# Kernel optimization log

Hardware: AMD Instinct MI355X
Metric: run time of the kernel (lower is better)

Reference implementation:

```python
import jax, jax.numpy as jnp
import numpy as np

# GraphVToS (keras) faithful jax reference.
# Original math: for every atom pair (i,j), concat(vf[i], vf[j]) along features,
# project with w_vs [2F,K] + b_vs, multiply by pairwise distance vector d[i,j,c],
# sum over coordinate axis c (=3), apply activation.
# We avoid materializing the [B,N,N,3,2F] tile by splitting w_vs into the halves
# acting on vf[i] and vf[j] (exact same linear map, distributivity of concat-matmul).

B, N, C, F, K = 8, 128, 3, 64, 64

def setup_inputs() -> dict:
    key = jax.random.key(0)
    k1, k2, k3 = jax.random.split(key, 3)
    vector_features = jax.random.normal(k1, (B, N, C, F), dtype=jnp.float32)
    distances = jax.random.normal(k2, (B, N, N, C), dtype=jnp.float32)
    w_vs = jax.random.normal(k3, (2 * F, K), dtype=jnp.float32) * (1.0 / np.sqrt(2 * F))
    b_vs = jnp.zeros((K,), dtype=jnp.float32)
    return {"vector_features": vector_features, "distances": distances,
            "w_vs": w_vs, "b_vs": b_vs}

def reference(vector_features, distances, w_vs, b_vs):
    f = vector_features.shape[-1]
    w_i, w_j = w_vs[:f], w_vs[f:]          # halves acting on vf[i] / vf[j]
    # Per-atom projections: [B,N,C,K]
    p_i = jnp.einsum('bncf,fk->bnck', vector_features, w_i)
    p_j = jnp.einsum('bncf,fk->bnck', vector_features, w_j)
    # Distance-weighted reduction over coordinate axis c -> [B,N,N,K]
    s = (jnp.einsum('bick,bijc->bijk', p_i, distances)
         + jnp.einsum('bjck,bijc->bijk', p_j, distances))
    # Bias contributes b_vs * sum_c d[i,j,c]
    s = s + distances.sum(axis=-1)[..., None] * b_vs
    return jax.nn.relu(s)
```

## Files before the change

kernel.cpp:

```cpp
#include <hip/hip_runtime.h>

#define Bz 8
#define Nz 128
#define Cz 3
#define Fz 64
#define Kz 64

__global__ __launch_bounds__(256) void proj_kernel(const float* __restrict__ vf,
                                                   const float4* __restrict__ w4,
                                                   const float4* __restrict__ bv4,
                                                   float4* __restrict__ P4) {
    int idx = blockIdx.x * blockDim.x + threadIdx.x;
    const int PER4 = (Bz * Nz * Cz * Kz) / 4;
    int which = idx / PER4;
    int rem   = idx - which * PER4;
    int k4 = rem & 15;
    int c  = (rem >> 4) % Cz;
    int bn = rem / (Cz * Kz / 4);

    const float*  vrow = vf + (bn * Cz + c) * Fz;
    const float4* wcol = w4 + which * (Fz * Kz / 4) + k4;

    float4 acc = make_float4(0.f, 0.f, 0.f, 0.f);
    #pragma unroll 8
    for (int f = 0; f < Fz; ++f) {
        float v = vrow[f];
        float4 wv = wcol[f * 16];
        acc.x += v * wv.x; acc.y += v * wv.y; acc.z += v * wv.z; acc.w += v * wv.w;
    }
    if (which == 0) {
        float4 bv = bv4[k4];
        acc.x += bv.x; acc.y += bv.y; acc.z += bv.z; acc.w += bv.w;
    }
    P4[idx] = acc;
}

__global__ __launch_bounds__(256) void pair_kernel(const float* __restrict__ d,
                                                   const float4* __restrict__ P4,
                                                   float4* __restrict__ out4) {
    const int PER4 = (Bz * Nz * Cz * Kz) / 4;
    int t   = threadIdx.x;
    int k4  = t & 15;
    int jc  = (t >> 4) & 15;
    int i   = blockIdx.x & (Nz - 1);
    int b   = blockIdx.x >> 7;

    const float4* pi = P4 + (b * Nz + i) * 48 + k4;
    float4 a0 = pi[0], a1 = pi[16], a2 = pi[32];

    const float*  drow = d + ((b * Nz + i) * Nz) * Cz;
    const float4* pjb  = P4 + PER4 + (b * Nz) * 48 + k4;
    float4*       ob   = out4 + ((b * Nz + i) * Nz) * 16 + k4;

    #pragma unroll
    for (int jj = 0; jj < 8; ++jj) {
        int j = jc * 8 + jj;
        const float* dp = drow + j * 3;
        float d0 = dp[0], d1 = dp[1], d2 = dp[2];

        const float4* pj = pjb + j * 48;
        float4 c0 = pj[0], c1 = pj[16], c2 = pj[32];

        float4 r;
        r.x = fmaxf(d0 * (a0.x + c0.x) + d1 * (a1.x + c1.x) + d2 * (a2.x + c2.x), 0.f);
        r.y = fmaxf(d0 * (a0.y + c0.y) + d1 * (a1.y + c1.y) + d2 * (a2.y + c2.y), 0.f);
        r.z = fmaxf(d0 * (a0.z + c0.z) + d1 * (a1.z + c1.z) + d2 * (a2.z + c2.z), 0.f);
        r.w = fmaxf(d0 * (a0.w + c0.w) + d1 * (a1.w + c1.w) + d2 * (a2.w + c2.w), 0.f);
        ob[j * 16] = r;
    }
}

extern "C" void kernel_launch(void* const* d_in, const int* in_sizes, int n_in,
                              void* d_out, int out_size, void* d_ws, size_t ws_size,
                              hipStream_t stream) {
    const float* vf  = (const float*)d_in[0];
    const float* dst = (const float*)d_in[1];
    const float* w   = (const float*)d_in[2];
    const float* bvs = (const float*)d_in[3];
    float* out = (float*)d_out;
    float* P   = (float*)d_ws;

    proj_kernel<<<384, 256, 0, stream>>>(vf, (const float4*)w,
                                         (const float4*)bvs, (float4*)P);
    pair_kernel<<<Bz * Nz, 256, 0, stream>>>(dst, (const float4*)P, (float4*)out);
}
```

Before: 79.36 us.

## Stage distances in LDS, split j-range across two blocks, use nontemporal loads/stores

The pair kernel now launches twice as many blocks, each handling half of the j range (64 atoms) with 4 j per thread instead of 8. The distance row is loaded once per block into shared memory with vectorized nontemporal loads, replacing per-thread scalar global loads. Output writes use nontemporal stores to avoid polluting cache with the 32MB streaming output. The changes aim at better occupancy and memory efficiency, at the cost of a block-level barrier and duplicated loads of the i-side projections.

```diff
diff --git a/kernel.cpp b/kernel.cpp
--- a/kernel.cpp
+++ b/kernel.cpp
@@ -5,6 +5,8 @@
 #define Cz 3
 #define Fz 64
 #define Kz 64
+
+typedef float v4f __attribute__((ext_vector_type(4)));
 
 __global__ __launch_bounds__(256) void proj_kernel(const float* __restrict__ vf,
                                                    const float4* __restrict__ w4,
@@ -36,37 +38,47 @@
 }
 
 __global__ __launch_bounds__(256) void pair_kernel(const float* __restrict__ d,
-                                                   const float4* __restrict__ P4,
-                                                   float4* __restrict__ out4) {
+                                                   const v4f* __restrict__ P4,
+                                                   v4f* __restrict__ out4) {
     const int PER4 = (Bz * Nz * Cz * Kz) / 4;
-    int t   = threadIdx.x;
-    int k4  = t & 15;
-    int jc  = (t >> 4) & 15;
-    int i   = blockIdx.x & (Nz - 1);
-    int b   = blockIdx.x >> 7;
+    __shared__ float ds[64 * Cz];
 
-    const float4* pi = P4 + (b * Nz + i) * 48 + k4;
-    float4 a0 = pi[0], a1 = pi[16], a2 = pi[32];
+    int t  = threadIdx.x;
+    int bi = blockIdx.x >> 1;
+    int jh = blockIdx.x & 1;
+    int i  = bi & (Nz - 1);
+    int b  = bi >> 7;
 
-    const float*  drow = d + ((b * Nz + i) * Nz) * Cz;
-    const float4* pjb  = P4 + PER4 + (b * Nz) * 48 + k4;
-    float4*       ob   = out4 + ((b * Nz + i) * Nz) * 16 + k4;
+    const float* drow = d + ((b * Nz + i) * Nz + jh * 64) * Cz;
+    if (t < 48) {
+        ((v4f*)ds)[t] = __builtin_nontemporal_load((const v4f*)drow + t);
+    }
+
+    int k4 = t & 15;
+    int jg = (t >> 4) & 15;
+
+    const v4f* pi = P4 + (b * Nz + i) * 48 + k4;
+    v4f a0 = pi[0], a1 = pi[16], a2 = pi[32];
+
+    __syncthreads();
+
+    const v4f* pjb = P4 + PER4 + (b * Nz + jh * 64) * 48 + k4;
+    v4f*       ob  = out4 + ((b * Nz + i) * Nz + jh * 64) * 16 + k4;
 
     #pragma unroll
-    for (int jj = 0; jj < 8; ++jj) {
-        int j = jc * 8 + jj;
-        const float* dp = drow + j * 3;
-        float d0 = dp[0], d1 = dp[1], d2 = dp[2];
+    for (int jj = 0; jj < 4; ++jj) {
+        int jl = jg * 4 + jj;
+        float d0 = ds[jl * 3 + 0], d1 = ds[jl * 3 + 1], d2 = ds[jl * 3 + 2];
 
-        const float4* pj = pjb + j * 48;
-        float4 c0 = pj[0], c1 = pj[16], c2 = pj[32];
+        const v4f* pj = pjb + jl * 48;
+        v4f c0 = pj[0], c1 = pj[16], c2 = pj[32];
 
-        float4 r;
-        r.x = fmaxf(d0 * (a0.x + c0.x) + d1 * (a1.x + c1.x) + d2 * (a2.x + c2.x), 0.f);
-        r.y = fmaxf(d0 * (a0.y + c0.y) + d1 * (a1.y + c1.y) + d2 * (a2.y + c2.y), 0.f);
-        r.z = fmaxf(d0 * (a0.z + c0.z) + d1 * (a1.z + c1.z) + d2 * (a2.z + c2.z), 0.f);
-        r.w = fmaxf(d0 * (a0.w + c0.w) + d1 * (a1.w + c1.w) + d2 * (a2.w + c2.w), 0.f);
-        ob[j * 16] = r;
+        v4f r = d0 * (a0 + c0) + d1 * (a1 + c1) + d2 * (a2 + c2);
+        r.x = fmaxf(r.x, 0.f);
+        r.y = fmaxf(r.y, 0.f);
+        r.z = fmaxf(r.z, 0.f);
+        r.w = fmaxf(r.w, 0.f);
+        __builtin_nontemporal_store(r, ob + jl * 16);
     }
 }
 
@@ -82,5 +94,5 @@
 
     proj_kernel<<<384, 256, 0, stream>>>(vf, (const float4*)w,
                                          (const float4*)bvs, (float4*)P);
-    pair_kernel<<<Bz * Nz, 256, 0, stream>>>(dst, (const float4*)P, (float4*)out);
+    pair_kernel<<<Bz * Nz * 2, 256, 0, stream>>>(dst, (const v4f*)P, (v4f*)out);
 }
```

Result: no change. 80.53 us (+1.5%).
